# Optimization experiments

Hardware: AMD Instinct MI355X
Metric: run time of the kernel (lower is better)

Reference implementation:

```python
import jax, jax.numpy as jnp
import numpy as np

N_QUBITS = 12
DIM = 2 ** N_QUBITS
EPS = 1e-8


def _ry(st, theta, w):
    # st: complex tensor of shape (2,)*n; apply RY(theta) on wire w
    st = jnp.moveaxis(st, w, 0)
    h = theta * 0.5
    c, s = jnp.cos(h), jnp.sin(h)
    out = jnp.stack([c * st[0] - s * st[1], s * st[0] + c * st[1]])
    return jnp.moveaxis(out, 0, w)


def _crx(st, theta, ctrl, tgt):
    # controlled-RX(theta): RX on tgt when ctrl == 1
    st = jnp.moveaxis(st, (ctrl, tgt), (0, 1))
    h = theta * 0.5
    c, s = jnp.cos(h), jnp.sin(h)
    r10 = c * st[1, 0] - 1j * s * st[1, 1]
    r11 = -1j * s * st[1, 0] + c * st[1, 1]
    out = jnp.stack([st[0], jnp.stack([r10, r11])])
    return jnp.moveaxis(out, (0, 1), (ctrl, tgt))


def _ansatz14(params, state, n=N_QUBITS):
    # Sim et al. (2019) ansatz 14, 1 layer, 4*n params; matches PennyLane gate order
    st = state.reshape((2,) * n)
    for i in range(n):
        st = _ry(st, params[i], i)
    for k, i in enumerate(range(n - 1, -1, -1)):
        st = _crx(st, params[n + k], i, (i + 1) % n)
    for i in range(n):
        st = _ry(st, params[2 * n + i], i)
    order = [n - 1] + list(range(n - 1))
    for k, i in enumerate(order):
        st = _crx(st, params[3 * n + k], i, (i - 1) % n)
    return st.reshape(-1)


def _measure_xyz(state, n=N_QUBITS):
    # expvals of X, Y, Z on every wire (PennyLane order: all X, all Y, all Z)
    st = state.reshape((2,) * n)
    xs, ys, zs = [], [], []
    for w in range(n):
        sm = jnp.moveaxis(st, w, 0)
        z01 = jnp.sum(jnp.conj(sm[0]) * sm[1])
        xs.append(2.0 * jnp.real(z01))
        ys.append(2.0 * jnp.imag(z01))
        zs.append(jnp.sum(jnp.abs(sm[0]) ** 2 - jnp.abs(sm[1]) ** 2))
    return jnp.stack(xs + ys + zs).astype(jnp.float32)


def setup_inputs() -> dict:
    key = jax.random.key(0)
    ks = jax.random.split(key, 7)
    L, D = 1024, 512
    P = 4 * N_QUBITS  # n_pqc_params = 48
    return {
        "tokens_emb": jax.random.normal(ks[0], (L, D), jnp.float32),
        "W_ang": jax.random.normal(ks[1], (P, D), jnp.float32) * 0.02,
        "b_ang": jax.random.normal(ks[2], (P,), jnp.float32) * 0.02,
        "qsvt_coeffs": jax.random.normal(ks[3], (4,), jnp.float32) * 0.1,
        "lcu_re": jax.random.normal(ks[4], (L,), jnp.float32),
        "lcu_im": jax.random.normal(ks[5], (L,), jnp.float32),
        "ff_params": jax.random.normal(ks[6], (P,), jnp.float32),
    }


def reference(tokens_emb, W_ang, b_ang, qsvt_coeffs, lcu_re, lcu_im, ff_params):
    # angles per token: Linear(d_model -> 4*n_qubits)
    pqc_angles = tokens_emb @ W_ang.T + b_ang  # [L, 4n]
    lcu = (lcu_re + 1j * lcu_im).astype(jnp.complex64)
    lcu = lcu / jnp.maximum(jnp.sum(jnp.abs(lcu)), EPS)

    basis0 = jnp.zeros(DIM, jnp.complex64).at[0].set(1.0)
    evolve = jax.vmap(_ansatz14, in_axes=(0, None))  # over tokens

    def lcu_apply(phi):
        norm = jnp.linalg.norm(phi)
        small = norm < EPS
        norm_eff = jnp.where(small, 1.0, norm)
        init = jnp.where(small, basis0, phi / norm_eff)
        evolved = evolve(pqc_angles, init)  # [L, DIM] complex
        return norm_eff * jnp.einsum("t,td->d", lcu, evolved)

    acc = qsvt_coeffs[0] * basis0
    mono = basis0
    for k in range(1, qsvt_coeffs.shape[0]):  # qsvt_degree iterations
        mono = lcu_apply(mono)
        acc = acc + qsvt_coeffs[k] * mono

    acc = acc / jnp.maximum(jnp.sum(jnp.abs(qsvt_coeffs)), EPS)
    snorm = jnp.linalg.norm(acc)
    small = snorm < EPS
    ff_in = jnp.where(small, basis0, acc / jnp.where(small, 1.0, snorm))
    return _measure_xyz(_ansatz14(ff_params, ff_in))  # [3*n_qubits] float32
```

## Files before the change

### kernel.cpp

```cpp
#include <hip/hip_runtime.h>
#include <math.h>

#define EPSV 1e-8f
#define QDIM 4096
#define LTOK 1024
#define PPAR 48

__device__ __forceinline__ int phz(int i) { return i ^ ((i >> 4) & 15); }
__device__ __forceinline__ int swz(int c) { return c ^ ((c >> 4) & 15); }

__device__ constexpr int SB[8][4] = {
  {0, 1, 2, 11},
  {2, 3, 4, 5},
  {5, 6, 7, 8},
  {8, 9, 10, 11},
  {0, 1, 10, 11},
  {7, 8, 9, 10},
  {4, 5, 6, 7},
  {1, 2, 3, 4}};
__device__ constexpr int SNG[8] = {7, 6, 6, 5, 7, 6, 6, 5};
__device__ constexpr int SG[8][7][4] = {
  {{0,3,0,0},{0,2,0,9},{0,1,0,10},{0,0,0,11},{1,0,3,12},{1,1,0,13},{1,2,1,14}},
  {{0,3,0,6},{0,2,0,7},{0,1,0,8},{1,1,0,15},{1,2,1,16},{1,3,2,17},{0,0,0,0}},
  {{0,3,0,3},{0,2,0,4},{0,1,0,5},{1,1,0,18},{1,2,1,19},{1,3,2,20},{0,0,0,0}},
  {{0,2,0,1},{0,1,0,2},{1,1,0,21},{1,2,1,22},{1,3,2,23},{0,0,0,0},{0,0,0,0}},
  {{0,3,0,24},{0,2,0,25},{0,1,0,34},{0,0,0,35},{1,0,1,36},{1,3,0,37},{1,2,3,38}},
  {{0,2,0,26},{0,1,0,27},{0,0,0,28},{1,2,3,39},{1,1,2,40},{1,0,1,41},{0,0,0,0}},
  {{0,2,0,29},{0,1,0,30},{0,0,0,31},{1,2,3,42},{1,1,2,43},{1,0,1,44},{0,0,0,0}},
  {{0,2,0,32},{0,1,0,33},{1,2,3,45},{1,1,2,46},{1,0,1,47},{0,0,0,0},{0,0,0,0}}};

template <int S>
__device__ __forceinline__ int i0_expand(int tid) {
  int i = tid;
#pragma unroll
  for (int j = 0; j < 4; ++j) {
    const int p = SB[S][j];
    i = ((i & ~((1 << p) - 1)) << 1) | (i & ((1 << p) - 1));
  }
  return i;
}

__device__ __forceinline__ int mof(int s, int r) {
  return ((r & 1) << SB[s][0]) | (((r >> 1) & 1) << SB[s][1]) |
         (((r >> 2) & 1) << SB[s][2]) | (((r >> 3) & 1) << SB[s][3]);
}

template <int S>
__device__ __forceinline__ void lds_gather(const float2* st, int tid, float2 (&amp)[16]) {
  const int pz = phz(i0_expand<S>(tid));
#pragma unroll
  for (int r = 0; r < 16; ++r) amp[r] = st[pz ^ swz(mof(S, r))];
}

template <int S>
__device__ __forceinline__ void lds_scatter(float2* st, int tid, const float2 (&amp)[16]) {
  const int pz = phz(i0_expand<S>(tid));
#pragma unroll
  for (int r = 0; r < 16; ++r) st[pz ^ swz(mof(S, r))] = amp[r];
}

template <int S>
__device__ __forceinline__ void apply_stage(float2 (&amp)[16], const float2* prm) {
#pragma unroll
  for (int g = 0; g < SNG[S]; ++g) {
    const int ty = SG[S][g][0], ja = SG[S][g][1], jb = SG[S][g][2], pi = SG[S][g][3];
    const float2 w = prm[pi];
    const float cs = w.x, sn = w.y;
    if (ty == 0) {
#pragma unroll
      for (int r = 0; r < 16; ++r) {
        if (((r >> ja) & 1) == 0) {
          const int q = r | (1 << ja);
          const float2 a0 = amp[r], a1 = amp[q];
          amp[r] = make_float2(cs * a0.x - sn * a1.x, cs * a0.y - sn * a1.y);
          amp[q] = make_float2(sn * a0.x + cs * a1.x, sn * a0.y + cs * a1.y);
        }
      }
    } else {
#pragma unroll
      for (int r = 0; r < 16; ++r) {
        if ((((r >> ja) & 1) == 1) && (((r >> jb) & 1) == 0)) {
          const int q = r | (1 << jb);
          const float2 a0 = amp[r], a1 = amp[q];
          amp[r] = make_float2(fmaf(cs, a0.x,  sn * a1.y), fmaf(cs, a0.y, -sn * a1.x));
          amp[q] = make_float2(fmaf(cs, a1.x,  sn * a0.y), fmaf(cs, a1.y, -sn * a0.x));
        }
      }
    }
  }
}

template <int S, bool SCAT>
__device__ __forceinline__ void do_stage(float2* st, int tid, float2 (&amp)[16],
                                         const float2* prm) {
  __syncthreads();
  lds_gather<S>(st, tid, amp);
  apply_stage<S>(amp, prm);
  if (SCAT) lds_scatter<S>(st, tid, amp);
}

__device__ __forceinline__ float block_reduce_sum(float v, float* red, int tid) {
#pragma unroll
  for (int off = 32; off > 0; off >>= 1) v += __shfl_down(v, off, 64);
  __syncthreads();
  if ((tid & 63) == 0) red[tid >> 6] = v;
  __syncthreads();
  return red[0] + red[1] + red[2] + red[3];
}

__device__ __forceinline__ float3 block_reduce3(float a, float b, float c,
                                                float* red, int tid) {
#pragma unroll
  for (int off = 32; off > 0; off >>= 1) {
    a += __shfl_down(a, off, 64);
    b += __shfl_down(b, off, 64);
    c += __shfl_down(c, off, 64);
  }
  __syncthreads();
  if ((tid & 63) == 0) {
    const int w = tid >> 6;
    red[w] = a; red[4 + w] = b; red[8 + w] = c;
  }
  __syncthreads();
  return make_float3(red[0] + red[1] + red[2] + red[3],
                     red[4] + red[5] + red[6] + red[7],
                     red[8] + red[9] + red[10] + red[11]);
}

__global__ __launch_bounds__(64) void k_angles(
    const float* __restrict__ emb, const float* __restrict__ W,
    const float* __restrict__ b, float2* __restrict__ cssn) {
  __shared__ float4 e4[128];
  const int tid = threadIdx.x, t = blockIdx.x;
  const float4* E4 = (const float4*)(emb + (size_t)t * 512);
  e4[tid * 2] = E4[tid * 2];
  e4[tid * 2 + 1] = E4[tid * 2 + 1];
  __syncthreads();
  if (tid < PPAR) {
    const float4* W4 = (const float4*)(W + (size_t)tid * 512);
    float a = 0.f;
#pragma unroll 4
    for (int k = 0; k < 128; ++k) {
      const float4 wv = W4[k], ev = e4[k];
      a += wv.x * ev.x + wv.y * ev.y + wv.z * ev.z + wv.w * ev.w;
    }
    const float h = 0.5f * (a + b[tid]);
    float sn, cs;
    sincosf(h, &sn, &cs);
    cssn[t * PPAR + tid] = make_float2(cs, sn);
  }
}

__global__ __launch_bounds__(256) void k_init(
    const float* __restrict__ lre, const float* __restrict__ lim,
    const float* __restrict__ qc, const float* __restrict__ ffp,
    float* __restrict__ scal, float2* __restrict__ ffcs,
    float2* __restrict__ mono, float2* __restrict__ acc) {
  __shared__ float red[4];
  const int tid = threadIdx.x;
  float s = 0.f;
#pragma unroll
  for (int j = 0; j < 4; ++j) {
    const int t = tid + 256 * j;
    s += sqrtf(lre[t] * lre[t] + lim[t] * lim[t]);
  }
  const float tot = block_reduce_sum(s, red, tid);
  if (tid == 0) {
    scal[0] = fmaxf(tot, EPSV);
    scal[1] = fmaxf(fabsf(qc[0]) + fabsf(qc[1]) + fabsf(qc[2]) + fabsf(qc[3]), EPSV);
  }
  if (tid < PPAR) {
    const float h = 0.5f * ffp[tid];
    float sn, cs;
    sincosf(h, &sn, &cs);
    ffcs[tid] = make_float2(cs, sn);
  }
  const float q0 = qc[0];
#pragma unroll
  for (int j = 0; j < 16; ++j) {
    const int d = tid + 256 * j;
    mono[d] = make_float2(d == 0 ? 1.f : 0.f, 0.f);
    acc[d]  = make_float2(d == 0 ? q0 : 0.f, 0.f);
  }
}

__device__ __forceinline__ float load16_g(const float2* __restrict__ src, int i0,
                                          float2 (&amp)[16]) {
  const float4* a4 = (const float4*)(src + i0);
  const float4* b4 = (const float4*)(src + i0 + 2048);
  float nr = 0.f;
#pragma unroll
  for (int j = 0; j < 4; ++j) {
    const float4 va = a4[j], vb = b4[j];
    amp[2 * j]     = make_float2(va.x, va.y);
    amp[2 * j + 1] = make_float2(va.z, va.w);
    amp[8 + 2 * j]     = make_float2(vb.x, vb.y);
    amp[8 + 2 * j + 1] = make_float2(vb.z, vb.w);
    nr += va.x * va.x + va.y * va.y + va.z * va.z + va.w * va.w;
    nr += vb.x * vb.x + vb.y * vb.y + vb.z * vb.z + vb.w * vb.w;
  }
  return nr;
}

template <int TPB>
__global__ __launch_bounds__(256, 4) void k_evolve(
    const float2* __restrict__ cssn, const float* __restrict__ lre,
    const float* __restrict__ lim, const float* __restrict__ scal,
    const float2* __restrict__ mono, float2* __restrict__ partial) {
  __shared__ float2 st[QDIM];
  __shared__ float2 prm[PPAR];
  __shared__ float red[4];
  const int tid = threadIdx.x;
  const float lnorm = scal[0];
  float2 racc[16];
  if (TPB > 1) {
#pragma unroll
    for (int r = 0; r < 16; ++r) racc[r] = make_float2(0.f, 0.f);
  }

  for (int ti = 0; ti < TPB; ++ti) {
    const int t = blockIdx.x * TPB + ti;
    __syncthreads();
    if (tid < PPAR) prm[tid] = cssn[(size_t)t * PPAR + tid];

    const int i0 = i0_expand<0>(tid);
    float2 amp[16];
    float nr = load16_g(mono, i0, amp);
    const float tot = block_reduce_sum(nr, red, tid);
    if (tot < EPSV * EPSV) {
#pragma unroll
      for (int r = 0; r < 16; ++r)
        amp[r] = make_float2((tid == 0 && r == 0) ? 1.f : 0.f, 0.f);
    }
    apply_stage<0>(amp, prm);
    lds_scatter<0>(st, tid, amp);
    do_stage<1, true>(st, tid, amp, prm);
    do_stage<2, true>(st, tid, amp, prm);
    do_stage<3, true>(st, tid, amp, prm);
    do_stage<4, true>(st, tid, amp, prm);
    do_stage<5, true>(st, tid, amp, prm);
    do_stage<6, true>(st, tid, amp, prm);
    do_stage<7, false>(st, tid, amp, prm);

    const float wr = lre[t] / lnorm, wi = lim[t] / lnorm;
    if (TPB == 1) {
#pragma unroll
      for (int r = 0; r < 16; ++r)
        partial[(size_t)blockIdx.x * QDIM + r * 256 + tid] =
            make_float2(wr * amp[r].x - wi * amp[r].y, wr * amp[r].y + wi * amp[r].x);
    } else {
#pragma unroll
      for (int r = 0; r < 16; ++r) {
        racc[r].x += wr * amp[r].x - wi * amp[r].y;
        racc[r].y += wr * amp[r].y + wi * amp[r].x;
      }
    }
  }
  if (TPB > 1) {
#pragma unroll
    for (int r = 0; r < 16; ++r)
      partial[(size_t)blockIdx.x * QDIM + r * 256 + tid] = racc[r];
  }
}

__global__ __launch_bounds__(256) void k_fold(
    const float4* __restrict__ partial4, float4* __restrict__ partial24) {
  const int d = blockIdx.x * 256 + threadIdx.x;
  const int b0 = blockIdx.y * 16;
  float4 s = make_float4(0.f, 0.f, 0.f, 0.f);
#pragma unroll
  for (int b = 0; b < 16; ++b) {
    const float4 v = partial4[(size_t)(b0 + b) * 2048 + d];
    s.x += v.x; s.y += v.y; s.z += v.z; s.w += v.w;
  }
  partial24[(size_t)blockIdx.y * 2048 + d] = s;
}

__global__ __launch_bounds__(256) void k_update(
    const float4* __restrict__ partial24, int F, float4* __restrict__ mono4,
    float4* __restrict__ acc4, const float* __restrict__ qc, int k) {
  const int idx = blockIdx.x * 256 + threadIdx.x;
  float4 s = make_float4(0.f, 0.f, 0.f, 0.f);
  for (int f = 0; f < F; ++f) {
    const float4 v = partial24[(size_t)f * 2048 + idx];
    s.x += v.x; s.y += v.y; s.z += v.z; s.w += v.w;
  }
  const int p = idx * 2;
  const int t = p & 255, r = p >> 8;
  const int i = ((t & 254) << 4) | (r << 1);
  mono4[i >> 1] = s;
  const float q = qc[k];
  float4 a = acc4[i >> 1];
  a.x += q * s.x; a.y += q * s.y; a.z += q * s.z; a.w += q * s.w;
  acc4[i >> 1] = a;
}

__global__ __launch_bounds__(256) void k_final(
    const float2* __restrict__ acc, const float* __restrict__ scal,
    const float2* __restrict__ ffcs, float* __restrict__ out) {
  __shared__ float2 st[QDIM];
  __shared__ float2 prm[PPAR];
  __shared__ float red[12];
  const int tid = threadIdx.x;
  if (tid < PPAR) prm[tid] = ffcs[tid];

  const int i0 = i0_expand<0>(tid);
  float2 amp[16];
  float nr = load16_g(acc, i0, amp);
  const float na = sqrtf(block_reduce_sum(nr, red, tid));
  const float qsum = scal[1];
  const bool small = na < EPSV * qsum;
  const float inv = small ? 0.f : 1.f / na;
#pragma unroll
  for (int r = 0; r < 16; ++r) {
    if (small) amp[r] = make_float2((tid == 0 && r == 0) ? 1.f : 0.f, 0.f);
    else { amp[r].x *= inv; amp[r].y *= inv; }
  }
  apply_stage<0>(amp, prm);
  lds_scatter<0>(st, tid, amp);
  do_stage<1, true>(st, tid, amp, prm);
  do_stage<2, true>(st, tid, amp, prm);
  do_stage<3, true>(st, tid, amp, prm);
  do_stage<4, true>(st, tid, amp, prm);
  do_stage<5, true>(st, tid, amp, prm);
  do_stage<6, true>(st, tid, amp, prm);
  do_stage<7, true>(st, tid, amp, prm);
  __syncthreads();

  for (int w = 0; w < 12; ++w) {
    const int bt = 11 - w;
    const int m = (1 << bt) - 1;
    const int dlt = swz(1 << bt);
    float xr = 0.f, xi = 0.f, zz = 0.f;
#pragma unroll
    for (int it = 0; it < 8; ++it) {
      const int pp = tid + it * 256;
      const int ia = ((pp & ~m) << 1) | (pp & m);
      const int p0 = phz(ia), p1 = p0 ^ dlt;
      const float2 a0 = st[p0], a1 = st[p1];
      xr += a0.x * a1.x + a0.y * a1.y;
      xi += a0.x * a1.y - a0.y * a1.x;
      zz += a0.x * a0.x + a0.y * a0.y - a1.x * a1.x - a1.y * a1.y;
    }
    const float3 s3 = block_reduce3(xr, xi, zz, red, tid);
    if (tid == 0) { out[w] = 2.f * s3.x; out[12 + w] = 2.f * s3.y; out[24 + w] = s3.z; }
  }
}

extern "C" void kernel_launch(void* const* d_in, const int* in_sizes, int n_in,
                              void* d_out, int out_size, void* d_ws, size_t ws_size,
                              hipStream_t stream) {
  const float* emb = (const float*)d_in[0];
  const float* W   = (const float*)d_in[1];
  const float* bb  = (const float*)d_in[2];
  const float* qc  = (const float*)d_in[3];
  const float* lre = (const float*)d_in[4];
  const float* lim = (const float*)d_in[5];
  const float* ffp = (const float*)d_in[6];
  float* out = (float*)d_out;

  char* ws = (char*)d_ws;
  size_t off = 0;
  float2* cssn = (float2*)(ws + off); off += (size_t)LTOK * PPAR * 8;
  float* scal  = (float*)(ws + off);  off += 256;
  float2* ffcs = (float2*)(ws + off); off += 512;
  float2* mono = (float2*)(ws + off); off += (size_t)QDIM * 8;
  float2* acc  = (float2*)(ws + off); off += (size_t)QDIM * 8;
  const size_t base = off;

  auto need = [&](int NB) {
    return base + (size_t)NB * QDIM * 8 + (size_t)(NB / 16) * QDIM * 8;
  };
  int TPB;
  if (ws_size >= need(1024)) TPB = 1;
  else if (ws_size >= need(512)) TPB = 2;
  else if (ws_size >= need(256)) TPB = 4;
  else TPB = 16;
  const int NB = LTOK / TPB, F = NB / 16;
  float2* partial  = (float2*)(ws + base);
  float2* partial2 = (float2*)(ws + base + (size_t)NB * QDIM * 8);

  k_init<<<1, 256, 0, stream>>>(lre, lim, qc, ffp, scal, ffcs, mono, acc);
  k_angles<<<LTOK, 64, 0, stream>>>(emb, W, bb, cssn);
  for (int k = 1; k <= 3; ++k) {
    if (TPB == 1)
      k_evolve<1><<<NB, 256, 0, stream>>>(cssn, lre, lim, scal, mono, partial);
    else if (TPB == 2)
      k_evolve<2><<<NB, 256, 0, stream>>>(cssn, lre, lim, scal, mono, partial);
    else if (TPB == 4)
      k_evolve<4><<<NB, 256, 0, stream>>>(cssn, lre, lim, scal, mono, partial);
    else
      k_evolve<16><<<NB, 256, 0, stream>>>(cssn, lre, lim, scal, mono, partial);
    k_fold<<<dim3(8, F), 256, 0, stream>>>((const float4*)partial, (float4*)partial2);
    k_update<<<8, 256, 0, stream>>>((const float4*)partial2, F, (float4*)mono,
                                    (float4*)acc, qc, k);
  }
  k_final<<<1, 256, 0, stream>>>(acc, scal, ffcs, out);
}
```

Measured before the change: 268.8 us.

## Precompute mono norm in update kernel and split final measurement across blocks

The per-token block reduction of the input state norm inside k_evolve is removed. k_update now writes eight per-block partial norms, and k_evolve only sums those eight values. This drops one block-wide reduction and its barriers from every evolve block in each of the three iterations. The final kernel is also split: one block evolves the feed-forward state into a global buffer, and a new 12-block kernel computes the X/Y/Z expectations for all wires in parallel. The cost is an extra launch and a global round trip for the final state.

Result: faster. 259.1 us (-3.6%).

```diff
diff --git a/kernel.cpp b/kernel.cpp
--- a/kernel.cpp
+++ b/kernel.cpp
@@ -154,8 +154,9 @@
 __global__ __launch_bounds__(256) void k_init(
     const float* __restrict__ lre, const float* __restrict__ lim,
     const float* __restrict__ qc, const float* __restrict__ ffp,
-    float* __restrict__ scal, float2* __restrict__ ffcs,
-    float2* __restrict__ mono, float2* __restrict__ acc) {
+    float* __restrict__ scal, float* __restrict__ snrm,
+    float2* __restrict__ ffcs, float2* __restrict__ mono,
+    float2* __restrict__ acc) {
   __shared__ float red[4];
   const int tid = threadIdx.x;
   float s = 0.f;
@@ -169,6 +170,7 @@
     scal[0] = fmaxf(tot, EPSV);
     scal[1] = fmaxf(fabsf(qc[0]) + fabsf(qc[1]) + fabsf(qc[2]) + fabsf(qc[3]), EPSV);
   }
+  if (tid < 8) snrm[tid] = (tid == 0) ? 1.f : 0.f;
   if (tid < PPAR) {
     const float h = 0.5f * ffp[tid];
     float sn, cs;
@@ -206,28 +208,31 @@
 __global__ __launch_bounds__(256, 4) void k_evolve(
     const float2* __restrict__ cssn, const float* __restrict__ lre,
     const float* __restrict__ lim, const float* __restrict__ scal,
-    const float2* __restrict__ mono, float2* __restrict__ partial) {
+    const float* __restrict__ snrm, const float2* __restrict__ mono,
+    float2* __restrict__ partial) {
   __shared__ float2 st[QDIM];
   __shared__ float2 prm[PPAR];
-  __shared__ float red[4];
   const int tid = threadIdx.x;
   const float lnorm = scal[0];
+  const float m2 = snrm[0] + snrm[1] + snrm[2] + snrm[3] +
+                   snrm[4] + snrm[5] + snrm[6] + snrm[7];
+  const bool small = m2 < EPSV * EPSV;
   float2 racc[16];
   if (TPB > 1) {
 #pragma unroll
     for (int r = 0; r < 16; ++r) racc[r] = make_float2(0.f, 0.f);
   }
 
+  const int i0 = i0_expand<0>(tid);
   for (int ti = 0; ti < TPB; ++ti) {
     const int t = blockIdx.x * TPB + ti;
+    if (TPB > 1 && ti > 0) __syncthreads();
+    if (tid < PPAR) prm[tid] = cssn[(size_t)t * PPAR + tid];
+
+    float2 amp[16];
+    load16_g(mono, i0, amp);
     __syncthreads();
-    if (tid < PPAR) prm[tid] = cssn[(size_t)t * PPAR + tid];
-
-    const int i0 = i0_expand<0>(tid);
-    float2 amp[16];
-    float nr = load16_g(mono, i0, amp);
-    const float tot = block_reduce_sum(nr, red, tid);
-    if (tot < EPSV * EPSV) {
+    if (small) {
 #pragma unroll
       for (int r = 0; r < 16; ++r)
         amp[r] = make_float2((tid == 0 && r == 0) ? 1.f : 0.f, 0.f);
@@ -278,8 +283,11 @@
 
 __global__ __launch_bounds__(256) void k_update(
     const float4* __restrict__ partial24, int F, float4* __restrict__ mono4,
-    float4* __restrict__ acc4, const float* __restrict__ qc, int k) {
-  const int idx = blockIdx.x * 256 + threadIdx.x;
+    float4* __restrict__ acc4, const float* __restrict__ qc, int k,
+    float* __restrict__ snrm) {
+  __shared__ float red[4];
+  const int tid = threadIdx.x;
+  const int idx = blockIdx.x * 256 + tid;
   float4 s = make_float4(0.f, 0.f, 0.f, 0.f);
   for (int f = 0; f < F; ++f) {
     const float4 v = partial24[(size_t)f * 2048 + idx];
@@ -293,20 +301,23 @@
   float4 a = acc4[i >> 1];
   a.x += q * s.x; a.y += q * s.y; a.z += q * s.z; a.w += q * s.w;
   acc4[i >> 1] = a;
-}
-
-__global__ __launch_bounds__(256) void k_final(
+  const float nr = s.x * s.x + s.y * s.y + s.z * s.z + s.w * s.w;
+  const float bn = block_reduce_sum(nr, red, tid);
+  if (tid == 0) snrm[blockIdx.x] = bn;
+}
+
+__global__ __launch_bounds__(256) void k_ffevolve(
     const float2* __restrict__ acc, const float* __restrict__ scal,
-    const float2* __restrict__ ffcs, float* __restrict__ out) {
+    const float2* __restrict__ ffcs, float2* __restrict__ fstate) {
   __shared__ float2 st[QDIM];
   __shared__ float2 prm[PPAR];
-  __shared__ float red[12];
+  __shared__ float red[4];
   const int tid = threadIdx.x;
   if (tid < PPAR) prm[tid] = ffcs[tid];
 
   const int i0 = i0_expand<0>(tid);
   float2 amp[16];
-  float nr = load16_g(acc, i0, amp);
+  const float nr = load16_g(acc, i0, amp);
   const float na = sqrtf(block_reduce_sum(nr, red, tid));
   const float qsum = scal[1];
   const bool small = na < EPSV * qsum;
@@ -324,27 +335,31 @@
   do_stage<4, true>(st, tid, amp, prm);
   do_stage<5, true>(st, tid, amp, prm);
   do_stage<6, true>(st, tid, amp, prm);
-  do_stage<7, true>(st, tid, amp, prm);
-  __syncthreads();
-
-  for (int w = 0; w < 12; ++w) {
-    const int bt = 11 - w;
-    const int m = (1 << bt) - 1;
-    const int dlt = swz(1 << bt);
-    float xr = 0.f, xi = 0.f, zz = 0.f;
-#pragma unroll
-    for (int it = 0; it < 8; ++it) {
-      const int pp = tid + it * 256;
-      const int ia = ((pp & ~m) << 1) | (pp & m);
-      const int p0 = phz(ia), p1 = p0 ^ dlt;
-      const float2 a0 = st[p0], a1 = st[p1];
-      xr += a0.x * a1.x + a0.y * a1.y;
-      xi += a0.x * a1.y - a0.y * a1.x;
-      zz += a0.x * a0.x + a0.y * a0.y - a1.x * a1.x - a1.y * a1.y;
-    }
-    const float3 s3 = block_reduce3(xr, xi, zz, red, tid);
-    if (tid == 0) { out[w] = 2.f * s3.x; out[12 + w] = 2.f * s3.y; out[24 + w] = s3.z; }
-  }
+  do_stage<7, false>(st, tid, amp, prm);
+#pragma unroll
+  for (int r = 0; r < 16; ++r) fstate[r * 256 + tid] = amp[r];
+}
+
+__global__ __launch_bounds__(256) void k_meas(
+    const float2* __restrict__ fstate, float* __restrict__ out) {
+  __shared__ float red[12];
+  const int w = blockIdx.x;
+  const int b = 11 - w;
+  const int pd = (b == 0) ? 1 : ((b <= 4) ? (256 << (b - 1)) : (1 << (b - 4)));
+  const int m = pd - 1;
+  const int tid = threadIdx.x;
+  float xr = 0.f, xi = 0.f, zz = 0.f;
+#pragma unroll
+  for (int it = 0; it < 8; ++it) {
+    const int q = tid + it * 256;
+    const int p0 = ((q & ~m) << 1) | (q & m);
+    const float2 a0 = fstate[p0], a1 = fstate[p0 | pd];
+    xr += a0.x * a1.x + a0.y * a1.y;
+    xi += a0.x * a1.y - a0.y * a1.x;
+    zz += a0.x * a0.x + a0.y * a0.y - a1.x * a1.x - a1.y * a1.y;
+  }
+  const float3 s3 = block_reduce3(xr, xi, zz, red, tid);
+  if (tid == 0) { out[w] = 2.f * s3.x; out[12 + w] = 2.f * s3.y; out[24 + w] = s3.z; }
 }
 
 extern "C" void kernel_launch(void* const* d_in, const int* in_sizes, int n_in,
@@ -363,9 +378,11 @@
   size_t off = 0;
   float2* cssn = (float2*)(ws + off); off += (size_t)LTOK * PPAR * 8;
   float* scal  = (float*)(ws + off);  off += 256;
+  float* snrm  = (float*)(ws + off);  off += 256;
   float2* ffcs = (float2*)(ws + off); off += 512;
   float2* mono = (float2*)(ws + off); off += (size_t)QDIM * 8;
   float2* acc  = (float2*)(ws + off); off += (size_t)QDIM * 8;
+  float2* fstate = (float2*)(ws + off); off += (size_t)QDIM * 8;
   const size_t base = off;
 
   auto need = [&](int NB) {
@@ -380,20 +397,21 @@
   float2* partial  = (float2*)(ws + base);
   float2* partial2 = (float2*)(ws + base + (size_t)NB * QDIM * 8);
 
-  k_init<<<1, 256, 0, stream>>>(lre, lim, qc, ffp, scal, ffcs, mono, acc);
+  k_init<<<1, 256, 0, stream>>>(lre, lim, qc, ffp, scal, snrm, ffcs, mono, acc);
   k_angles<<<LTOK, 64, 0, stream>>>(emb, W, bb, cssn);
   for (int k = 1; k <= 3; ++k) {
     if (TPB == 1)
-      k_evolve<1><<<NB, 256, 0, stream>>>(cssn, lre, lim, scal, mono, partial);
+      k_evolve<1><<<NB, 256, 0, stream>>>(cssn, lre, lim, scal, snrm, mono, partial);
     else if (TPB == 2)
-      k_evolve<2><<<NB, 256, 0, stream>>>(cssn, lre, lim, scal, mono, partial);
+      k_evolve<2><<<NB, 256, 0, stream>>>(cssn, lre, lim, scal, snrm, mono, partial);
     else if (TPB == 4)
-      k_evolve<4><<<NB, 256, 0, stream>>>(cssn, lre, lim, scal, mono, partial);
+      k_evolve<4><<<NB, 256, 0, stream>>>(cssn, lre, lim, scal, snrm, mono, partial);
     else
-      k_evolve<16><<<NB, 256, 0, stream>>>(cssn, lre, lim, scal, mono, partial);
+      k_evolve<16><<<NB, 256, 0, stream>>>(cssn, lre, lim, scal, snrm, mono, partial);
     k_fold<<<dim3(8, F), 256, 0, stream>>>((const float4*)partial, (float4*)partial2);
     k_update<<<8, 256, 0, stream>>>((const float4*)partial2, F, (float4*)mono,
-                                    (float4*)acc, qc, k);
-  }
-  k_final<<<1, 256, 0, stream>>>(acc, scal, ffcs, out);
-}
+                                    (float4*)acc, qc, k, snrm);
+  }
+  k_ffevolve<<<1, 256, 0, stream>>>(acc, scal, ffcs, fstate);
+  k_meas<<<12, 256, 0, stream>>>(fstate, out);
+}
```
